# Optimization experiments

Measured on AMD Instinct MI355X. Metric: run time of the kernel, lower is better.

## Reference

```python
import jax, jax.numpy as jnp
import numpy as np

B, I, H, O, K = 256, 512, 512, 512, 256


def setup_inputs() -> dict:
    key = jax.random.key(0)
    ks = jax.random.split(key, 16)
    def lin(kw, kb, out_dim, in_dim):
        s = 1.0 / np.sqrt(in_dim)
        W = jax.random.uniform(kw, (out_dim, in_dim), jnp.float32, -s, s)
        b = jax.random.uniform(kb, (out_dim,), jnp.float32, -s, s)
        return W, b
    Wd, bd = lin(ks[0], ks[1], H, I + 2 * H)
    Wr, br = lin(ks[2], ks[3], H, I + H)
    Wz, bz = lin(ks[4], ks[5], H, I + H)
    Wh, bh = lin(ks[6], ks[7], H, I + H)
    Wo, bo = lin(ks[8], ks[9], O, H)
    return {
        "sample": jax.random.normal(ks[10], (B, I), jnp.float32),
        "hidden": jax.random.normal(ks[11], (B, H), jnp.float32),
        "hidden_tensor": jax.random.normal(ks[12], (K, B, H), jnp.float32),
        "d_0": jax.random.normal(ks[13], (B, H), jnp.float32),
        "Wd": Wd, "bd": bd, "Wr": Wr, "br": br,
        "Wz": Wz, "bz": bz, "Wh": Wh, "bh": bh, "Wo": Wo, "bo": bo,
    }


def _filter_d(hidden_tensor, d_values):
    # get_ws: w[j] = prod_{m=0}^{K-1-j} (m - d) / (m + 1)  for j in [0, K)
    # Vectorized: cumprod of (m-d)/(m+1) along m, then flip.
    m = jnp.arange(K, dtype=d_values.dtype).reshape(K, 1, 1)  # [K,1,1]
    factors = (m - d_values[None, :, :]) / (m + 1.0)          # [K,B,H]
    w = jnp.flip(jnp.cumprod(factors, axis=0), axis=0)        # [K,B,H]
    return jnp.sum(hidden_tensor * w, axis=0)                 # [B,H]


def reference(sample, hidden, hidden_tensor, d_0,
              Wd, bd, Wr, br, Wz, bz, Wh, bh, Wo, bo):
    combined = jnp.concatenate([sample, hidden], axis=1)          # [B, I+H]
    combined_d = jnp.concatenate([sample, hidden, d_0], axis=1)   # [B, I+2H]

    d_values = jax.nn.sigmoid(combined_d @ Wd.T + bd) * 0.5       # [B,H]
    first = -_filter_d(hidden_tensor, d_values)                   # [B,H]

    r_gate = jax.nn.sigmoid(combined @ Wr.T + br)
    z_gate = jax.nn.sigmoid(combined @ Wz.T + bz)

    combined2 = jnp.concatenate([sample, r_gate * hidden], axis=1)
    h_tilde = jnp.tanh(combined2 @ Wh.T + bh)
    second = h_tilde * (1.0 - z_gate)

    hidden_new = first + second                                   # [B,H]
    h_c_1 = jnp.concatenate([hidden_tensor, hidden_new[None]], axis=0)[1:]  # [K,B,H]
    output = hidden_new @ Wo.T + bo                               # [B,O]
    return (output, hidden_new, h_c_1, d_values)
```

## Files before the change

kernel.cpp:

```cpp
#include <hip/hip_runtime.h>

#define B_ 256
#define I_ 512
#define H_ 512
#define O_ 512
#define KF 256
#define BH 131072

#define BM 64
#define BN 64
#define BK 16

__device__ __forceinline__ float sigmoidf_(float x) { return 1.0f / (1.0f + __expf(-x)); }
__device__ __forceinline__ float tanh_fast(float x) { return 2.0f / (1.0f + __expf(-2.0f * x)) - 1.0f; }


#define MAC_LOOP()                                                         \
    _Pragma("unroll")                                                      \
    for (int kk = 0; kk < BK; ++kk) {                                      \
        const float4 a = *(const float4*)&As[kk][ty << 2];                 \
        const float4 w = *(const float4*)&Ws[kk][tx << 2];                 \
        const float a4[4] = {a.x, a.y, a.z, a.w};                          \
        const float w4[4] = {w.x, w.y, w.z, w.w};                          \
        _Pragma("unroll")                                                  \
        for (int i = 0; i < 4; ++i)                                        \
            _Pragma("unroll")                                              \
            for (int j = 0; j < 4; ++j)                                    \
                acc[i][j] = fmaf(a4[i], w4[j], acc[i][j]);                 \
    }

#define STORE_TILE()                                                       \
    As[lcol + 0][lrow] = av.x; As[lcol + 1][lrow] = av.y;                  \
    As[lcol + 2][lrow] = av.z; As[lcol + 3][lrow] = av.w;                  \
    Ws[lcol + 0][lrow] = wv.x; Ws[lcol + 1][lrow] = wv.y;                  \
    Ws[lcol + 2][lrow] = wv.z; Ws[lcol + 3][lrow] = wv.w;

__global__ __launch_bounds__(256) void gemm_drz_part(
    const float* __restrict__ sample, const float* __restrict__ hidden,
    const float* __restrict__ d0,
    const float* __restrict__ Wd, const float* __restrict__ Wr,
    const float* __restrict__ Wz,
    float* __restrict__ parts)
{
    __shared__ float As[BK][BM + 4];
    __shared__ float Ws[BK][BN + 4];

    const int z = blockIdx.z;
    int gemm, s;
    if (z < 6)       { gemm = 0; s = z; }
    else if (z < 10) { gemm = 1; s = z - 6; }
    else             { gemm = 2; s = z - 10; }
    const int Ktot = (gemm == 0) ? 1536 : 1024;
    const float* __restrict__ W = (gemm == 0) ? Wd : ((gemm == 1) ? Wr : Wz);
    const int ks  = s << 8;
    const int seg = ks >> 9;
    const float* abase = (seg == 0) ? sample : ((seg == 1) ? hidden : d0);
    const int aoff = ks & 511;

    const int tid = threadIdx.x;
    const int bm = blockIdx.y * BM, bn = blockIdx.x * BN;
    const int ty = tid >> 4, tx = tid & 15;
    const int lrow = tid >> 2, lcol = (tid & 3) << 2;

    const float* aptr = abase + (bm + lrow) * 512 + aoff + lcol;
    const float* wptr = W + (size_t)(bn + lrow) * Ktot + ks + lcol;

    float acc[4][4] = {};
    float4 av = *(const float4*)aptr;
    float4 wv = *(const float4*)wptr;

    for (int it = 0; it < 16; ++it) {
        __syncthreads();
        STORE_TILE();
        __syncthreads();
        if (it < 15) {
            av = *(const float4*)(aptr + (it + 1) * BK);
            wv = *(const float4*)(wptr + (it + 1) * BK);
        }
        MAC_LOOP();
    }

    float* p = parts + (size_t)z * BH;
    #pragma unroll
    for (int i = 0; i < 4; ++i) {
        const int m = bm + (ty << 2) + i;
        #pragma unroll
        for (int j = 0; j < 4; ++j)
            p[m * H_ + bn + (tx << 2) + j] = acc[i][j];
    }
}

__global__ __launch_bounds__(256) void reduce_drz(
    const float* __restrict__ parts,
    const float* __restrict__ bd, const float* __restrict__ br,
    const float* __restrict__ bz,
    float* __restrict__ dv, float* __restrict__ rb, float* __restrict__ zb)
{
    const int g = blockIdx.x * 256 + threadIdx.x;
    const int n = g & (H_ - 1);
    float sd = bd[n], sr = br[n], sz = bz[n];
    #pragma unroll
    for (int s = 0; s < 6; ++s) sd += parts[(size_t)s * BH + g];
    #pragma unroll
    for (int s = 0; s < 4; ++s) sr += parts[(size_t)(6 + s) * BH + g];
    #pragma unroll
    for (int s = 0; s < 4; ++s) sz += parts[(size_t)(10 + s) * BH + g];
    dv[g] = 0.5f * sigmoidf_(sd);
    rb[g] = sigmoidf_(sr);
    zb[g] = sigmoidf_(sz);
}

__global__ __launch_bounds__(256) void gemm_h_part(
    const float* __restrict__ sample, const float* __restrict__ hidden,
    const float* __restrict__ rb, const float* __restrict__ Wh,
    float* __restrict__ parts)
{
    __shared__ float As[BK][BM + 4];
    __shared__ float Ws[BK][BN + 4];

    const int z = blockIdx.z;
    const int ks = z << 8;
    const bool mul = (ks >= 512);
    const int aoff = ks & 511;

    const int tid = threadIdx.x;
    const int bm = blockIdx.y * BM, bn = blockIdx.x * BN;
    const int ty = tid >> 4, tx = tid & 15;
    const int lrow = tid >> 2, lcol = (tid & 3) << 2;

    const float* aptr = (mul ? hidden : sample) + (bm + lrow) * 512 + aoff + lcol;
    const float* rptr = rb + (bm + lrow) * 512 + aoff + lcol;
    const float* wptr = Wh + (size_t)(bn + lrow) * 1024 + ks + lcol;

    float acc[4][4] = {};
    float4 av = *(const float4*)aptr;
    if (mul) {
        const float4 rv = *(const float4*)rptr;
        av.x *= rv.x; av.y *= rv.y; av.z *= rv.z; av.w *= rv.w;
    }
    float4 wv = *(const float4*)wptr;

    for (int it = 0; it < 16; ++it) {
        __syncthreads();
        STORE_TILE();
        __syncthreads();
        if (it < 15) {
            av = *(const float4*)(aptr + (it + 1) * BK);
            if (mul) {
                const float4 rv = *(const float4*)(rptr + (it + 1) * BK);
                av.x *= rv.x; av.y *= rv.y; av.z *= rv.z; av.w *= rv.w;
            }
            wv = *(const float4*)(wptr + (it + 1) * BK);
        }
        MAC_LOOP();
    }

    float* p = parts + (size_t)z * BH;
    #pragma unroll
    for (int i = 0; i < 4; ++i) {
        const int m = bm + (ty << 2) + i;
        #pragma unroll
        for (int j = 0; j < 4; ++j)
            p[m * H_ + bn + (tx << 2) + j] = acc[i][j];
    }
}

__global__ __launch_bounds__(256) void reduce_h(
    const float* __restrict__ parts, const float* __restrict__ bh,
    const float* __restrict__ zb, float* __restrict__ sec)
{
    const int g = blockIdx.x * 256 + threadIdx.x;
    const int n = g & (H_ - 1);
    float sh = bh[n];
    #pragma unroll
    for (int s = 0; s < 4; ++s) sh += parts[(size_t)s * BH + g];
    sec[g] = tanh_fast(sh) * (1.0f - zb[g]);
}

__global__ __launch_bounds__(256) void gemm_o_part(
    const float* __restrict__ hn, const float* __restrict__ Wo,
    float* __restrict__ parts, int NS)
{
    __shared__ float As[BK][BM + 4];
    __shared__ float Ws[BK][BN + 4];

    const int z = blockIdx.z;
    const int chunk = 512 / NS;
    const int nIter = chunk / BK;
    const int ks = z * chunk;

    const int tid = threadIdx.x;
    const int bm = blockIdx.y * BM, bn = blockIdx.x * BN;
    const int ty = tid >> 4, tx = tid & 15;
    const int lrow = tid >> 2, lcol = (tid & 3) << 2;

    const float* aptr = hn + (bm + lrow) * 512 + ks + lcol;
    const float* wptr = Wo + (size_t)(bn + lrow) * 512 + ks + lcol;

    float acc[4][4] = {};
    float4 av = *(const float4*)aptr;
    float4 wv = *(const float4*)wptr;

    for (int it = 0; it < nIter; ++it) {
        __syncthreads();
        STORE_TILE();
        __syncthreads();
        if (it < nIter - 1) {
            av = *(const float4*)(aptr + (it + 1) * BK);
            wv = *(const float4*)(wptr + (it + 1) * BK);
        }
        MAC_LOOP();
    }

    float* p = parts + (size_t)z * BH;
    #pragma unroll
    for (int i = 0; i < 4; ++i) {
        const int m = bm + (ty << 2) + i;
        #pragma unroll
        for (int j = 0; j < 4; ++j)
            p[m * O_ + bn + (tx << 2) + j] = acc[i][j];
    }
}

__global__ __launch_bounds__(256) void reduce_o(
    const float* parts, const float* __restrict__ bo, float* out, int NS)
{
    const int g = blockIdx.x * 256 + threadIdx.x;
    float v = bo[g & (O_ - 1)];
    for (int s = 0; s < NS; ++s) v += parts[(size_t)s * BH + g];
    out[g] = v;
}

__global__ __launch_bounds__(256) void filter_fuse(
    const float* __restrict__ ht, const float* __restrict__ dv,
    const float* sec, float* hc1, float* __restrict__ hn_out)
{
    __shared__ float s_inv[KF];
    __shared__ float s_tinv[KF];
    const int tid = threadIdx.x;
    const float finv = 1.0f / (float)(tid + 1);
    s_inv[tid]  = finv;
    s_tinv[tid] = (float)tid * finv;
    __syncthreads();

    const int g = blockIdx.x * 256 + tid;
    const float d   = dv[g];
    const float s2  = sec[g];
    float c = 1.0f, acc = 0.0f;

    #pragma unroll 8
    for (int t = 0; t < KF; ++t) {
        const int k = KF - 1 - t;
        const float v = ht[(size_t)k * BH + g];
        c *= fmaf(-d, s_inv[t], s_tinv[t]);
        acc = fmaf(v, c, acc);
        if (k >= 1) hc1[(size_t)(k - 1) * BH + g] = v;
    }

    const float hn = s2 - acc;
    hc1[(size_t)(KF - 1) * BH + g] = hn;
    hn_out[g] = hn;
}

extern "C" void kernel_launch(void* const* d_in, const int* in_sizes, int n_in,
                              void* d_out, int out_size, void* d_ws, size_t ws_size,
                              hipStream_t stream)
{
    const float* sample = (const float*)d_in[0];
    const float* hidden = (const float*)d_in[1];
    const float* ht     = (const float*)d_in[2];
    const float* d0     = (const float*)d_in[3];
    const float* Wd = (const float*)d_in[4];
    const float* bd = (const float*)d_in[5];
    const float* Wr = (const float*)d_in[6];
    const float* br = (const float*)d_in[7];
    const float* Wz = (const float*)d_in[8];
    const float* bz = (const float*)d_in[9];
    const float* Wh = (const float*)d_in[10];
    const float* bh = (const float*)d_in[11];
    const float* Wo = (const float*)d_in[12];
    const float* bo = (const float*)d_in[13];

    float* out     = (float*)d_out;
    float* out_o   = out;
    float* out_hn  = out + BH;
    float* out_hc1 = out + 2 * BH;
    float* out_dv  = out + 2 * BH + (size_t)KF * BH;

    float* sl = out_hc1;
    float* rb  = sl + (size_t)14 * BH;
    float* zb  = sl + (size_t)15 * BH;
    float* hp  = sl + (size_t)16 * BH;
    float* sec = sl + (size_t)20 * BH;

    gemm_drz_part<<<dim3(8, 4, 14), 256, 0, stream>>>(sample, hidden, d0,
                                                      Wd, Wr, Wz, sl);
    reduce_drz<<<dim3(BH / 256), 256, 0, stream>>>(sl, bd, br, bz,
                                                   out_dv, rb, zb);
    gemm_h_part<<<dim3(8, 4, 4), 256, 0, stream>>>(sample, hidden, rb, Wh, hp);
    reduce_h<<<dim3(BH / 256), 256, 0, stream>>>(hp, bh, zb, sec);
    filter_fuse<<<dim3(BH / 256), 256, 0, stream>>>(ht, out_dv, sec,
                                                    out_hc1, out_hn);

    const size_t needO = 4ull * BH * sizeof(float);
    if (ws_size >= needO) {
        float* op = (float*)d_ws;
        gemm_o_part<<<dim3(8, 4, 4), 256, 0, stream>>>(out_hn, Wo, op, 4);
        reduce_o<<<dim3(BH / 256), 256, 0, stream>>>(op, bo, out_o, 4);
    } else {
        gemm_o_part<<<dim3(8, 4, 1), 256, 0, stream>>>(out_hn, Wo, out_o, 1);
        reduce_o<<<dim3(BH / 256), 256, 0, stream>>>(out_o, bo, out_o, 1);
    }
}
```

Baseline: 100.8 us.

## Overlap fractional filter with gate GEMMs by splitting filter into two fused mega-kernels

The d-gate GEMM now runs first. The memory-bound fractional filter over hidden_tensor is split into two halves, each launched in the same grid as the r/z GEMM and the h GEMM respectively, so bandwidth-heavy filter blocks run alongside compute-bound GEMM blocks. The filter state (running product and accumulator) is carried between kernels through workspace buffers, and the reductions and finalisation are vectorised with float4. This adds workspace traffic and heterogeneous blocks in one grid, and it depends on a large enough workspace, otherwise it falls back to a sequential path.

```diff
diff --git a/kernel.cpp b/kernel.cpp
--- a/kernel.cpp
+++ b/kernel.cpp
@@ -1,11 +1,11 @@
 #include <hip/hip_runtime.h>
 
 #define B_ 256
-#define I_ 512
 #define H_ 512
-#define O_ 512
 #define KF 256
 #define BH 131072
+#define BH4 32768
+#define H4 128
 
 #define BM 64
 #define BN 64
@@ -13,241 +13,275 @@
 
 __device__ __forceinline__ float sigmoidf_(float x) { return 1.0f / (1.0f + __expf(-x)); }
 __device__ __forceinline__ float tanh_fast(float x) { return 2.0f / (1.0f + __expf(-2.0f * x)) - 1.0f; }
-
-
-#define MAC_LOOP()                                                         \
-    _Pragma("unroll")                                                      \
-    for (int kk = 0; kk < BK; ++kk) {                                      \
-        const float4 a = *(const float4*)&As[kk][ty << 2];                 \
-        const float4 w = *(const float4*)&Ws[kk][tx << 2];                 \
-        const float a4[4] = {a.x, a.y, a.z, a.w};                          \
-        const float w4[4] = {w.x, w.y, w.z, w.w};                          \
-        _Pragma("unroll")                                                  \
-        for (int i = 0; i < 4; ++i)                                        \
-            _Pragma("unroll")                                              \
-            for (int j = 0; j < 4; ++j)                                    \
-                acc[i][j] = fmaf(a4[i], w4[j], acc[i][j]);                 \
-    }
-
-#define STORE_TILE()                                                       \
-    As[lcol + 0][lrow] = av.x; As[lcol + 1][lrow] = av.y;                  \
-    As[lcol + 2][lrow] = av.z; As[lcol + 3][lrow] = av.w;                  \
-    Ws[lcol + 0][lrow] = wv.x; Ws[lcol + 1][lrow] = wv.y;                  \
-    Ws[lcol + 2][lrow] = wv.z; Ws[lcol + 3][lrow] = wv.w;
-
-__global__ __launch_bounds__(256) void gemm_drz_part(
-    const float* __restrict__ sample, const float* __restrict__ hidden,
-    const float* __restrict__ d0,
-    const float* __restrict__ Wd, const float* __restrict__ Wr,
-    const float* __restrict__ Wz,
-    float* __restrict__ parts)
-{
-    __shared__ float As[BK][BM + 4];
-    __shared__ float Ws[BK][BN + 4];
-
-    const int z = blockIdx.z;
-    int gemm, s;
-    if (z < 6)       { gemm = 0; s = z; }
-    else if (z < 10) { gemm = 1; s = z - 6; }
-    else             { gemm = 2; s = z - 10; }
-    const int Ktot = (gemm == 0) ? 1536 : 1024;
-    const float* __restrict__ W = (gemm == 0) ? Wd : ((gemm == 1) ? Wr : Wz);
-    const int ks  = s << 8;
-    const int seg = ks >> 9;
-    const float* abase = (seg == 0) ? sample : ((seg == 1) ? hidden : d0);
-    const int aoff = ks & 511;
-
+__device__ __forceinline__ float4 sig4(float4 v) {
+    return make_float4(sigmoidf_(v.x), sigmoidf_(v.y), sigmoidf_(v.z), sigmoidf_(v.w));
+}
+
+template<bool MUL>
+__device__ __forceinline__ void gemm64(
+    float (*As)[BM + 4], float (*Ws)[BN + 4],
+    const float* __restrict__ abase, const float* __restrict__ rbase,
+    const float* __restrict__ W, int Ktot, int ks,
+    int bm, int bn, int nIter, float* __restrict__ p)
+{
     const int tid = threadIdx.x;
-    const int bm = blockIdx.y * BM, bn = blockIdx.x * BN;
     const int ty = tid >> 4, tx = tid & 15;
     const int lrow = tid >> 2, lcol = (tid & 3) << 2;
-
-    const float* aptr = abase + (bm + lrow) * 512 + aoff + lcol;
+    const float* aptr = abase + (bm + lrow) * 512 + lcol;
+    const float* rptr = MUL ? rbase + (bm + lrow) * 512 + lcol : nullptr;
     const float* wptr = W + (size_t)(bn + lrow) * Ktot + ks + lcol;
 
     float acc[4][4] = {};
     float4 av = *(const float4*)aptr;
+    if (MUL) { const float4 rv = *(const float4*)rptr;
+               av.x *= rv.x; av.y *= rv.y; av.z *= rv.z; av.w *= rv.w; }
     float4 wv = *(const float4*)wptr;
 
-    for (int it = 0; it < 16; ++it) {
+    for (int it = 0; it < nIter; ++it) {
         __syncthreads();
-        STORE_TILE();
+        As[lcol + 0][lrow] = av.x; As[lcol + 1][lrow] = av.y;
+        As[lcol + 2][lrow] = av.z; As[lcol + 3][lrow] = av.w;
+        Ws[lcol + 0][lrow] = wv.x; Ws[lcol + 1][lrow] = wv.y;
+        Ws[lcol + 2][lrow] = wv.z; Ws[lcol + 3][lrow] = wv.w;
         __syncthreads();
-        if (it < 15) {
+        if (it < nIter - 1) {
             av = *(const float4*)(aptr + (it + 1) * BK);
+            if (MUL) { const float4 rv = *(const float4*)(rptr + (it + 1) * BK);
+                       av.x *= rv.x; av.y *= rv.y; av.z *= rv.z; av.w *= rv.w; }
             wv = *(const float4*)(wptr + (it + 1) * BK);
         }
-        MAC_LOOP();
-    }
-
-    float* p = parts + (size_t)z * BH;
+        #pragma unroll
+        for (int kk = 0; kk < BK; ++kk) {
+            const float4 a = *(const float4*)&As[kk][ty << 2];
+            const float4 w = *(const float4*)&Ws[kk][tx << 2];
+            const float a4[4] = {a.x, a.y, a.z, a.w};
+            const float w4[4] = {w.x, w.y, w.z, w.w};
+            #pragma unroll
+            for (int i = 0; i < 4; ++i)
+                #pragma unroll
+                for (int j = 0; j < 4; ++j)
+                    acc[i][j] = fmaf(a4[i], w4[j], acc[i][j]);
+        }
+    }
     #pragma unroll
     for (int i = 0; i < 4; ++i) {
         const int m = bm + (ty << 2) + i;
         #pragma unroll
         for (int j = 0; j < 4; ++j)
-            p[m * H_ + bn + (tx << 2) + j] = acc[i][j];
-    }
-}
-
-__global__ __launch_bounds__(256) void reduce_drz(
-    const float* __restrict__ parts,
-    const float* __restrict__ bd, const float* __restrict__ br,
-    const float* __restrict__ bz,
-    float* __restrict__ dv, float* __restrict__ rb, float* __restrict__ zb)
+            p[m * 512 + bn + (tx << 2) + j] = acc[i][j];
+    }
+}
+
+__global__ __launch_bounds__(256) void k_gemm_d(
+    const float* __restrict__ sample, const float* __restrict__ hidden,
+    const float* __restrict__ d0, const float* __restrict__ Wd,
+    float* __restrict__ parts)
+{
+    __shared__ float As[BK][BM + 4];
+    __shared__ float Ws[BK][BN + 4];
+    const int s = blockIdx.z, ks = s << 8, seg = ks >> 9;
+    const float* ab = (seg == 0 ? sample : (seg == 1 ? hidden : d0)) + (ks & 511);
+    gemm64<false>(As, Ws, ab, nullptr, Wd, 1536, ks,
+                  blockIdx.y * BM, blockIdx.x * BN, 16, parts + (size_t)s * BH);
+}
+
+__global__ __launch_bounds__(256) void k_mega1(
+    const float* __restrict__ ht, const float* dparts, const float* __restrict__ bd,
+    const float* __restrict__ sample, const float* __restrict__ hidden,
+    const float* __restrict__ Wr, const float* __restrict__ Wz,
+    float* __restrict__ rzparts, float* __restrict__ dv_out,
+    float* hc1, float* __restrict__ cst, float* __restrict__ accst)
+{
+    if (blockIdx.x >= 512) {
+        __shared__ float As[BK][BM + 4];
+        __shared__ float Ws[BK][BN + 4];
+        const int id = blockIdx.x - 512;
+        const int gz = id >> 7, rem = id & 127;
+        const int s = rem >> 5, t2 = rem & 31;
+        const int bn = (t2 >> 2) << 6, bm = (t2 & 3) << 6, ks = s << 8;
+        const float* ab = (ks < 512 ? sample + ks : hidden + (ks - 512));
+        gemm64<false>(As, Ws, ab, nullptr, gz ? Wz : Wr, 1024, ks, bm, bn, 16,
+                      rzparts + (size_t)(gz * 4 + s) * BH);
+        return;
+    }
+    __shared__ float s_inv[128], s_tinv[128];
+    const int tid = threadIdx.x;
+    if (tid < 128) { const float fi = 1.0f / (float)(tid + 1);
+                     s_inv[tid] = fi; s_tinv[tid] = (float)tid * fi; }
+    __syncthreads();
+
+    const int g = blockIdx.x * 256 + tid;
+    const int n = g & (H_ - 1);
+    float sd = bd[n];
+    #pragma unroll
+    for (int s = 0; s < 6; ++s) sd += dparts[(size_t)s * BH + g];
+    const float d = 0.5f * sigmoidf_(sd);
+    dv_out[g] = d;
+
+    float c = 1.0f, acc = 0.0f;
+    #pragma unroll 8
+    for (int t = 0; t < 128; ++t) {
+        const int k = 255 - t;
+        const float v = ht[(size_t)k * BH + g];
+        c *= fmaf(-d, s_inv[t], s_tinv[t]);
+        acc = fmaf(v, c, acc);
+        hc1[(size_t)(k - 1) * BH + g] = v;
+    }
+    cst[g] = c; accst[g] = acc;
+}
+
+__global__ __launch_bounds__(256) void k_reduce_rz(
+    const float4* __restrict__ parts, const float4* __restrict__ br,
+    const float4* __restrict__ bz, float4* __restrict__ rb, float4* __restrict__ zb)
 {
     const int g = blockIdx.x * 256 + threadIdx.x;
-    const int n = g & (H_ - 1);
-    float sd = bd[n], sr = br[n], sz = bz[n];
-    #pragma unroll
-    for (int s = 0; s < 6; ++s) sd += parts[(size_t)s * BH + g];
-    #pragma unroll
-    for (int s = 0; s < 4; ++s) sr += parts[(size_t)(6 + s) * BH + g];
-    #pragma unroll
-    for (int s = 0; s < 4; ++s) sz += parts[(size_t)(10 + s) * BH + g];
-    dv[g] = 0.5f * sigmoidf_(sd);
-    rb[g] = sigmoidf_(sr);
-    zb[g] = sigmoidf_(sz);
-}
-
-__global__ __launch_bounds__(256) void gemm_h_part(
+    const int n = g & (H4 - 1);
+    float4 r = br[n], z = bz[n];
+    #pragma unroll
+    for (int s = 0; s < 4; ++s) { const float4 p = parts[(size_t)s * BH4 + g];
+        r.x += p.x; r.y += p.y; r.z += p.z; r.w += p.w; }
+    #pragma unroll
+    for (int s = 4; s < 8; ++s) { const float4 p = parts[(size_t)s * BH4 + g];
+        z.x += p.x; z.y += p.y; z.z += p.z; z.w += p.w; }
+    rb[g] = sig4(r); zb[g] = sig4(z);
+}
+
+__global__ __launch_bounds__(256) void k_mega2(
+    const float* __restrict__ ht, const float* __restrict__ dv,
+    const float* __restrict__ sample, const float* __restrict__ hidden,
+    const float* __restrict__ rb, const float* __restrict__ Wh,
+    float* __restrict__ hparts, float* hc1,
+    const float* __restrict__ cst, float* __restrict__ accst)
+{
+    if (blockIdx.x >= 512) {
+        __shared__ float As[BK][BM + 4];
+        __shared__ float Ws[BK][BN + 4];
+        const int id = blockIdx.x - 512;
+        const int s = id >> 5, t2 = id & 31;
+        const int bn = (t2 >> 2) << 6, bm = (t2 & 3) << 6, ks = s << 8;
+        if (ks < 512)
+            gemm64<false>(As, Ws, sample + ks, nullptr, Wh, 1024, ks, bm, bn, 16,
+                          hparts + (size_t)s * BH);
+        else
+            gemm64<true>(As, Ws, hidden + (ks - 512), rb + (ks - 512), Wh, 1024, ks,
+                         bm, bn, 16, hparts + (size_t)s * BH);
+        return;
+    }
+    __shared__ float s_inv[128], s_tinv[128];
+    const int tid = threadIdx.x;
+    if (tid < 128) { const int t = tid + 128; const float fi = 1.0f / (float)(t + 1);
+                     s_inv[tid] = fi; s_tinv[tid] = (float)t * fi; }
+    __syncthreads();
+
+    const int g = blockIdx.x * 256 + tid;
+    const float d = dv[g];
+    float c = cst[g], acc = accst[g];
+    #pragma unroll 8
+    for (int t = 0; t < 128; ++t) {
+        const int k = 127 - t;
+        const float v = ht[(size_t)k * BH + g];
+        c *= fmaf(-d, s_inv[t], s_tinv[t]);
+        acc = fmaf(v, c, acc);
+        if (k >= 1) hc1[(size_t)(k - 1) * BH + g] = v;
+    }
+    accst[g] = acc;
+}
+
+__global__ __launch_bounds__(256) void k_finalize(
+    const float4* __restrict__ hparts, const float4* __restrict__ bh,
+    const float4* __restrict__ zb, const float4* __restrict__ accst,
+    float4* __restrict__ hn_out, float4* __restrict__ hc1_4)
+{
+    const int g = blockIdx.x * 256 + threadIdx.x;
+    const int n = g & (H4 - 1);
+    float4 sh = bh[n];
+    #pragma unroll
+    for (int s = 0; s < 4; ++s) { const float4 p = hparts[(size_t)s * BH4 + g];
+        sh.x += p.x; sh.y += p.y; sh.z += p.z; sh.w += p.w; }
+    const float4 z = zb[g], a = accst[g];
+    float4 hn;
+    hn.x = tanh_fast(sh.x) * (1.0f - z.x) - a.x;
+    hn.y = tanh_fast(sh.y) * (1.0f - z.y) - a.y;
+    hn.z = tanh_fast(sh.z) * (1.0f - z.z) - a.z;
+    hn.w = tanh_fast(sh.w) * (1.0f - z.w) - a.w;
+    hn_out[g] = hn;
+    hc1_4[(size_t)255 * BH4 + g] = hn;
+}
+
+__global__ __launch_bounds__(256) void k_gemm_o(
+    const float* __restrict__ hn, const float* __restrict__ Wo,
+    float* __restrict__ parts, int chunk)
+{
+    __shared__ float As[BK][BM + 4];
+    __shared__ float Ws[BK][BN + 4];
+    const int s = blockIdx.z, ks = s * chunk;
+    gemm64<false>(As, Ws, hn + ks, nullptr, Wo, 512, ks,
+                  blockIdx.y * BM, blockIdx.x * BN, chunk / BK, parts + (size_t)s * BH);
+}
+
+__global__ __launch_bounds__(256) void k_reduce_o(
+    const float4* parts, const float4* __restrict__ bo, float4* out, int NS)
+{
+    const int g = blockIdx.x * 256 + threadIdx.x;
+    float4 v = bo[g & (H4 - 1)];
+    for (int s = 0; s < NS; ++s) { const float4 p = parts[(size_t)s * BH4 + g];
+        v.x += p.x; v.y += p.y; v.z += p.z; v.w += p.w; }
+    out[g] = v;
+}
+
+__global__ __launch_bounds__(256) void k_gemm_rz(
+    const float* __restrict__ sample, const float* __restrict__ hidden,
+    const float* __restrict__ Wr, const float* __restrict__ Wz,
+    float* __restrict__ parts)
+{
+    __shared__ float As[BK][BM + 4];
+    __shared__ float Ws[BK][BN + 4];
+    const int z = blockIdx.z, gz = z >> 2, s = z & 3, ks = s << 8;
+    const float* ab = (ks < 512 ? sample + ks : hidden + (ks - 512));
+    gemm64<false>(As, Ws, ab, nullptr, gz ? Wz : Wr, 1024, ks,
+                  blockIdx.y * BM, blockIdx.x * BN, 16, parts + (size_t)z * BH);
+}
+
+__global__ __launch_bounds__(256) void k_gemm_h(
     const float* __restrict__ sample, const float* __restrict__ hidden,
     const float* __restrict__ rb, const float* __restrict__ Wh,
     float* __restrict__ parts)
 {
     __shared__ float As[BK][BM + 4];
     __shared__ float Ws[BK][BN + 4];
-
-    const int z = blockIdx.z;
-    const int ks = z << 8;
-    const bool mul = (ks >= 512);
-    const int aoff = ks & 511;
-
+    const int s = blockIdx.z, ks = s << 8;
+    if (ks < 512)
+        gemm64<false>(As, Ws, sample + ks, nullptr, Wh, 1024, ks,
+                      blockIdx.y * BM, blockIdx.x * BN, 16, parts + (size_t)s * BH);
+    else
+        gemm64<true>(As, Ws, hidden + (ks - 512), rb + (ks - 512), Wh, 1024, ks,
+                     blockIdx.y * BM, blockIdx.x * BN, 16, parts + (size_t)s * BH);
+}
+
+__global__ __launch_bounds__(256) void k_filter_full(
+    const float* __restrict__ ht, const float* dparts, const float* __restrict__ bd,
+    const float* zbuf, const float* hparts, const float* __restrict__ bh,
+    float* hc1, float* __restrict__ dv_out, float* __restrict__ hn_out)
+{
+    __shared__ float s_inv[KF], s_tinv[KF];
     const int tid = threadIdx.x;
-    const int bm = blockIdx.y * BM, bn = blockIdx.x * BN;
-    const int ty = tid >> 4, tx = tid & 15;
-    const int lrow = tid >> 2, lcol = (tid & 3) << 2;
-
-    const float* aptr = (mul ? hidden : sample) + (bm + lrow) * 512 + aoff + lcol;
-    const float* rptr = rb + (bm + lrow) * 512 + aoff + lcol;
-    const float* wptr = Wh + (size_t)(bn + lrow) * 1024 + ks + lcol;
-
-    float acc[4][4] = {};
-    float4 av = *(const float4*)aptr;
-    if (mul) {
-        const float4 rv = *(const float4*)rptr;
-        av.x *= rv.x; av.y *= rv.y; av.z *= rv.z; av.w *= rv.w;
-    }
-    float4 wv = *(const float4*)wptr;
-
-    for (int it = 0; it < 16; ++it) {
-        __syncthreads();
-        STORE_TILE();
-        __syncthreads();
-        if (it < 15) {
-            av = *(const float4*)(aptr + (it + 1) * BK);
-            if (mul) {
-                const float4 rv = *(const float4*)(rptr + (it + 1) * BK);
-                av.x *= rv.x; av.y *= rv.y; av.z *= rv.z; av.w *= rv.w;
-            }
-            wv = *(const float4*)(wptr + (it + 1) * BK);
-        }
-        MAC_LOOP();
-    }
-
-    float* p = parts + (size_t)z * BH;
-    #pragma unroll
-    for (int i = 0; i < 4; ++i) {
-        const int m = bm + (ty << 2) + i;
-        #pragma unroll
-        for (int j = 0; j < 4; ++j)
-            p[m * H_ + bn + (tx << 2) + j] = acc[i][j];
-    }
-}
-
-__global__ __launch_bounds__(256) void reduce_h(
-    const float* __restrict__ parts, const float* __restrict__ bh,
-    const float* __restrict__ zb, float* __restrict__ sec)
-{
-    const int g = blockIdx.x * 256 + threadIdx.x;
+    const float fi = 1.0f / (float)(tid + 1);
+    s_inv[tid] = fi; s_tinv[tid] = (float)tid * fi;
+    __syncthreads();
+
+    const int g = blockIdx.x * 256 + tid;
     const int n = g & (H_ - 1);
+    float sd = bd[n];
+    #pragma unroll
+    for (int s = 0; s < 6; ++s) sd += dparts[(size_t)s * BH + g];
+    const float d = 0.5f * sigmoidf_(sd);
+    dv_out[g] = d;
     float sh = bh[n];
     #pragma unroll
-    for (int s = 0; s < 4; ++s) sh += parts[(size_t)s * BH + g];
-    sec[g] = tanh_fast(sh) * (1.0f - zb[g]);
-}
-
-__global__ __launch_bounds__(256) void gemm_o_part(
-    const float* __restrict__ hn, const float* __restrict__ Wo,
-    float* __restrict__ parts, int NS)
-{
-    __shared__ float As[BK][BM + 4];
-    __shared__ float Ws[BK][BN + 4];
-
-    const int z = blockIdx.z;
-    const int chunk = 512 / NS;
-    const int nIter = chunk / BK;
-    const int ks = z * chunk;
-
-    const int tid = threadIdx.x;
-    const int bm = blockIdx.y * BM, bn = blockIdx.x * BN;
-    const int ty = tid >> 4, tx = tid & 15;
-    const int lrow = tid >> 2, lcol = (tid & 3) << 2;
-
-    const float* aptr = hn + (bm + lrow) * 512 + ks + lcol;
-    const float* wptr = Wo + (size_t)(bn + lrow) * 512 + ks + lcol;
-
-    float acc[4][4] = {};
-    float4 av = *(const float4*)aptr;
-    float4 wv = *(const float4*)wptr;
-
-    for (int it = 0; it < nIter; ++it) {
-        __syncthreads();
-        STORE_TILE();
-        __syncthreads();
-        if (it < nIter - 1) {
-            av = *(const float4*)(aptr + (it + 1) * BK);
-            wv = *(const float4*)(wptr + (it + 1) * BK);
-        }
-        MAC_LOOP();
-    }
-
-    float* p = parts + (size_t)z * BH;
-    #pragma unroll
-    for (int i = 0; i < 4; ++i) {
-        const int m = bm + (ty << 2) + i;
-        #pragma unroll
-        for (int j = 0; j < 4; ++j)
-            p[m * O_ + bn + (tx << 2) + j] = acc[i][j];
-    }
-}
-
-__global__ __launch_bounds__(256) void reduce_o(
-    const float* parts, const float* __restrict__ bo, float* out, int NS)
-{
-    const int g = blockIdx.x * 256 + threadIdx.x;
-    float v = bo[g & (O_ - 1)];
-    for (int s = 0; s < NS; ++s) v += parts[(size_t)s * BH + g];
-    out[g] = v;
-}
-
-__global__ __launch_bounds__(256) void filter_fuse(
-    const float* __restrict__ ht, const float* __restrict__ dv,
-    const float* sec, float* hc1, float* __restrict__ hn_out)
-{
-    __shared__ float s_inv[KF];
-    __shared__ float s_tinv[KF];
-    const int tid = threadIdx.x;
-    const float finv = 1.0f / (float)(tid + 1);
-    s_inv[tid]  = finv;
-    s_tinv[tid] = (float)tid * finv;
-    __syncthreads();
-
-    const int g = blockIdx.x * 256 + tid;
-    const float d   = dv[g];
-    const float s2  = sec[g];
+    for (int s = 0; s < 4; ++s) sh += hparts[(size_t)s * BH + g];
+    const float z = zbuf[g];
+
     float c = 1.0f, acc = 0.0f;
-
     #pragma unroll 8
     for (int t = 0; t < KF; ++t) {
         const int k = KF - 1 - t;
@@ -256,8 +290,7 @@
         acc = fmaf(v, c, acc);
         if (k >= 1) hc1[(size_t)(k - 1) * BH + g] = v;
     }
-
-    const float hn = s2 - acc;
+    const float hn = tanh_fast(sh) * (1.0f - z) - acc;
     hc1[(size_t)(KF - 1) * BH + g] = hn;
     hn_out[g] = hn;
 }
@@ -272,8 +305,8 @@
     const float* d0     = (const float*)d_in[3];
     const float* Wd = (const float*)d_in[4];
     const float* bd = (const float*)d_in[5];
+    const float* br = (const float*)d_in[7];
     const float* Wr = (const float*)d_in[6];
-    const float* br = (const float*)d_in[7];
     const float* Wz = (const float*)d_in[8];
     const float* bz = (const float*)d_in[9];
     const float* Wh = (const float*)d_in[10];
@@ -287,28 +320,48 @@
     float* out_hc1 = out + 2 * BH;
     float* out_dv  = out + 2 * BH + (size_t)KF * BH;
 
-    float* sl = out_hc1;
-    float* rb  = sl + (size_t)14 * BH;
-    float* zb  = sl + (size_t)15 * BH;
-    float* hp  = sl + (size_t)16 * BH;
-    float* sec = sl + (size_t)20 * BH;
-
-    gemm_drz_part<<<dim3(8, 4, 14), 256, 0, stream>>>(sample, hidden, d0,
-                                                      Wd, Wr, Wz, sl);
-    reduce_drz<<<dim3(BH / 256), 256, 0, stream>>>(sl, bd, br, bz,
-                                                   out_dv, rb, zb);
-    gemm_h_part<<<dim3(8, 4, 4), 256, 0, stream>>>(sample, hidden, rb, Wh, hp);
-    reduce_h<<<dim3(BH / 256), 256, 0, stream>>>(hp, bh, zb, sec);
-    filter_fuse<<<dim3(BH / 256), 256, 0, stream>>>(ht, out_dv, sec,
-                                                    out_hc1, out_hn);
-
-    const size_t needO = 4ull * BH * sizeof(float);
-    if (ws_size >= needO) {
-        float* op = (float*)d_ws;
-        gemm_o_part<<<dim3(8, 4, 4), 256, 0, stream>>>(out_hn, Wo, op, 4);
-        reduce_o<<<dim3(BH / 256), 256, 0, stream>>>(op, bo, out_o, 4);
+    const size_t slice = BH;
+    const size_t need = 12ull * slice * sizeof(float);
+
+    if (ws_size >= need) {
+        float* ws  = (float*)d_ws;
+        float* rz  = ws;
+        float* hp  = ws;
+        float* op  = ws + 4 * slice;
+        float* rb  = ws + 8 * slice;
+        float* zb  = ws + 9 * slice;
+        float* cst = ws + 10 * slice;
+        float* acc = ws + 11 * slice;
+        float* dpar = out_hc1;
+
+        k_gemm_d<<<dim3(8, 4, 6), 256, 0, stream>>>(sample, hidden, d0, Wd, dpar);
+        k_mega1<<<dim3(768), 256, 0, stream>>>(ht, dpar, bd, sample, hidden, Wr, Wz,
+                                               rz, out_dv, out_hc1, cst, acc);
+        k_reduce_rz<<<dim3(128), 256, 0, stream>>>((const float4*)rz, (const float4*)br,
+                                                   (const float4*)bz, (float4*)rb, (float4*)zb);
+        k_mega2<<<dim3(640), 256, 0, stream>>>(ht, out_dv, sample, hidden, rb, Wh,
+                                               hp, out_hc1, cst, acc);
+        k_finalize<<<dim3(128), 256, 0, stream>>>((const float4*)hp, (const float4*)bh,
+                                                  (const float4*)zb, (const float4*)acc,
+                                                  (float4*)out_hn, (float4*)out_hc1);
+        k_gemm_o<<<dim3(8, 4, 4), 256, 0, stream>>>(out_hn, Wo, op, 128);
+        k_reduce_o<<<dim3(128), 256, 0, stream>>>((const float4*)op, (const float4*)bo,
+                                                  (float4*)out_o, 4);
     } else {
-        gemm_o_part<<<dim3(8, 4, 1), 256, 0, stream>>>(out_hn, Wo, out_o, 1);
-        reduce_o<<<dim3(BH / 256), 256, 0, stream>>>(out_o, bo, out_o, 1);
-    }
-}
+        float* sl = out_hc1;
+        k_gemm_d<<<dim3(8, 4, 6), 256, 0, stream>>>(sample, hidden, d0, Wd, sl);
+        k_gemm_rz<<<dim3(8, 4, 8), 256, 0, stream>>>(sample, hidden, Wr, Wz, sl + 6 * slice);
+        k_reduce_rz<<<dim3(128), 256, 0, stream>>>((const float4*)(sl + 6 * slice),
+                                                   (const float4*)br, (const float4*)bz,
+                                                   (float4*)(sl + 14 * slice),
+                                                   (float4*)(sl + 15 * slice));
+        k_gemm_h<<<dim3(8, 4, 4), 256, 0, stream>>>(sample, hidden, sl + 14 * slice, Wh,
+                                                    sl + 16 * slice);
+        k_filter_full<<<dim3(512), 256, 0, stream>>>(ht, sl, bd, sl + 15 * slice,
+                                                     sl + 16 * slice, bh,
+                                                     out_hc1, out_dv, out_hn);
+        k_gemm_o<<<dim3(8, 4, 1), 256, 0, stream>>>(out_hn, Wo, out_o, 512);
+        k_reduce_o<<<dim3(128), 256, 0, stream>>>((const float4*)out_o, (const float4*)bo,
+                                                  (float4*)out_o, 1);
+    }
+}
```

Measured after the change: 89.92 us. 10.8% less time.
